# Performance work log

Hardware: AMD Instinct MI355X
Metric: run time of the kernel (lower is better)

The kernel has to match this reference:

```python
import jax, jax.numpy as jnp
import numpy as np

B, T, IN, H, OUT = 2048, 512, 6, 32, 64


def setup_inputs() -> dict:
    key = jax.random.key(0)
    ks = jax.random.split(key, 13)
    s_in = 1.0 / np.sqrt(H)  # torch LSTM/Linear default uniform bound
    u = lambda k, shape, s: jax.random.uniform(k, shape, jnp.float32, -s, s)
    return {
        "imu": jax.random.normal(ks[0], (B, T, IN), jnp.float32),
        # layer 0 (input_size=6)
        "w_ih0": u(ks[1], (4 * H, IN), s_in),
        "w_hh0": u(ks[2], (4 * H, H), s_in),
        "b_ih0": u(ks[3], (4 * H,), s_in),
        "b_hh0": u(ks[4], (4 * H,), s_in),
        # layer 1 (input_size=32)
        "w_ih1": u(ks[5], (4 * H, H), s_in),
        "w_hh1": u(ks[6], (4 * H, H), s_in),
        "b_ih1": u(ks[7], (4 * H,), s_in),
        "b_hh1": u(ks[8], (4 * H,), s_in),
        # heads
        "wf": u(ks[9], (OUT, H), s_in),
        "bf": u(ks[10], (OUT,), s_in),
        "wn": u(ks[11], (OUT, H), s_in),
        "bn": u(ks[12], (OUT,), s_in),
    }


def _lstm_layer(x, w_ih, w_hh, b_ih, b_hh):
    # x: [B, T, in] -> h sequence [B, T, H]; torch gate order: i, f, g, o
    b = x.shape[0]
    # precompute input contribution once: [B, T, 4H]
    gx = jnp.einsum("bti,gi->btg", x, w_ih) + b_ih + b_hh

    def step(carry, g_t):
        h, c = carry
        gates = g_t + h @ w_hh.T  # [B, 4H]
        i = jax.nn.sigmoid(gates[:, :H])
        f = jax.nn.sigmoid(gates[:, H:2 * H])
        g = jnp.tanh(gates[:, 2 * H:3 * H])
        o = jax.nn.sigmoid(gates[:, 3 * H:])
        c = f * c + i * g
        h = o * jnp.tanh(c)
        return (h, c), h

    h0 = jnp.zeros((b, H), x.dtype)
    (_, _), hs = jax.lax.scan(step, (h0, h0), jnp.swapaxes(gx, 0, 1))
    return jnp.swapaxes(hs, 0, 1)  # [B, T, H]


def reference(imu, w_ih0, w_hh0, b_ih0, b_hh0, w_ih1, w_hh1, b_ih1, b_hh1, wf, bf, wn, bn):
    h = _lstm_layer(imu, w_ih0, w_hh0, b_ih0, b_hh0)
    h = _lstm_layer(h, w_ih1, w_hh1, b_ih1, b_hh1)
    last = h[:, -1, :]  # [B, H]
    a_i = last @ wf.T + bf
    R_i = jnp.exp(last @ wn.T + bn)
    return (a_i, R_i)
```

## Files before the change

kernel.cpp:

```cpp
#include <hip/hip_runtime.h>

#define TT 512
#define BPB 8
#define NBLK (2048 / BPB)
#define OUTD 64

typedef __attribute__((ext_vector_type(8))) short short8;
typedef __attribute__((ext_vector_type(4))) float f32x4;

__device__ __forceinline__ short f2bf(float x) {
    union { float f; unsigned u; } v; v.f = x;
    unsigned r = (v.u + 0x7FFFu + ((v.u >> 16) & 1u)) >> 16;
    return (short)r;
}
__device__ __forceinline__ float sigm(float x) {
    return __builtin_amdgcn_rcpf(1.f + __expf(-x));
}
__device__ __forceinline__ float tanh_fast(float x) {
    return 2.f * sigm(2.f * x) - 1.f;
}

#define ACT_UPDATE(acc, c, hval)                                   \
    {                                                              \
        float gi = sigm((acc)[0]);                                 \
        float gf = sigm((acc)[1]);                                 \
        float gg = tanh_fast((acc)[2]);                            \
        float go = sigm((acc)[3]);                                 \
        (c) = gf * (c) + gi * gg;                                  \
        (hval) = go * tanh_fast((c));                              \
    }

__global__ __launch_bounds__(512, 1) void lstm2_inlane_kernel(
    const float* __restrict__ imu,
    const float* __restrict__ w_ih0, const float* __restrict__ w_hh0,
    const float* __restrict__ b_ih0, const float* __restrict__ b_hh0,
    const float* __restrict__ w_ih1, const float* __restrict__ w_hh1,
    const float* __restrict__ b_ih1, const float* __restrict__ b_hh1,
    const float* __restrict__ wf, const float* __restrict__ bf,
    const float* __restrict__ wn, const float* __restrict__ bn,
    float* __restrict__ out)
{
    const int tid   = threadIdx.x;
    const int l     = tid & 63;
    const int w     = tid >> 6;
    const int layer = w >> 2;
    const int pair  = w & 3;
    const int col   = l & 15;
    const int kg    = l >> 4;

    __shared__ __align__(16) short xfrag[TT][8][8];
    __shared__ __align__(16) short h1f[2][16][40];
    __shared__ __align__(16) short h2f[2][16][40];
    __shared__ __align__(16) float lasth[16][36];

    {
        short* p1 = &h1f[0][0][0];
        short* p2 = &h2f[0][0][0];
        for (int i = tid; i < 2 * 16 * 40; i += 512) { p1[i] = 0; p2[i] = 0; }
    }

    {
        const int bg0 = blockIdx.x * BPB;
        for (int p = tid; p < BPB * TT; p += 512) {
            const int b = p >> 9;
            const int t = p & (TT - 1);
            const float* src = imu + ((size_t)(bg0 + b) * TT + t) * 6;
            float2 a0 = *(const float2*)(src);
            float2 a1 = *(const float2*)(src + 2);
            float2 a2 = *(const float2*)(src + 4);
            unsigned* dst = (unsigned*)&xfrag[t][b][0];
            dst[0] = (unsigned short)f2bf(a0.x) | ((unsigned)(unsigned short)f2bf(a0.y) << 16);
            dst[1] = (unsigned short)f2bf(a1.x) | ((unsigned)(unsigned short)f2bf(a1.y) << 16);
            dst[2] = (unsigned short)f2bf(a2.x) | ((unsigned)(unsigned short)f2bf(a2.y) << 16);
            dst[3] = 0u;
        }
    }

    const int t0 = pair * 2, t1 = t0 + 1;
    const int m  = col;
    const int G0 = (m & 3) * 32 + t0 * 4 + (m >> 2);
    const int G1 = (m & 3) * 32 + t1 * 4 + (m >> 2);
    const int u0 = pair * 8 + kg;
    const int u1 = u0 + 4;

    short8 A00, A01, A10, A11;
    f32x4 bias0, bias1;
    if (layer == 0) {
        #pragma unroll
        for (int j = 0; j < 8; ++j) {
            A00[j] = (kg == 0 && j < 6) ? f2bf(w_ih0[G0 * 6 + j]) : (short)0;
            A10[j] = (kg == 0 && j < 6) ? f2bf(w_ih0[G1 * 6 + j]) : (short)0;
            A01[j] = f2bf(w_hh0[G0 * 32 + kg * 8 + j]);
            A11[j] = f2bf(w_hh0[G1 * 32 + kg * 8 + j]);
        }
        #pragma unroll
        for (int r = 0; r < 4; ++r) {
            bias0[r] = b_ih0[r * 32 + u0] + b_hh0[r * 32 + u0];
            bias1[r] = b_ih0[r * 32 + u1] + b_hh0[r * 32 + u1];
        }
    } else {
        #pragma unroll
        for (int j = 0; j < 8; ++j) {
            A00[j] = f2bf(w_ih1[G0 * 32 + kg * 8 + j]);
            A10[j] = f2bf(w_ih1[G1 * 32 + kg * 8 + j]);
            A01[j] = f2bf(w_hh1[G0 * 32 + kg * 8 + j]);
            A11[j] = f2bf(w_hh1[G1 * 32 + kg * 8 + j]);
        }
        #pragma unroll
        for (int r = 0; r < 4; ++r) {
            bias0[r] = b_ih1[r * 32 + u0] + b_hh1[r * 32 + u0];
            bias1[r] = b_ih1[r * 32 + u1] + b_hh1[r * 32 + u1];
        }
    }

    float c0 = 0.f, c1 = 0.f;

    const int xb = l & 7;
    const short8* h1r0  = (const short8*)&h1f[0][col][kg * 8];
    const short8* h1r1  = (const short8*)&h1f[1][col][kg * 8];
    const short8* h2r0  = (const short8*)&h2f[0][col][kg * 8];
    const short8* h2r1  = (const short8*)&h2f[1][col][kg * 8];

    __syncthreads();

    if (layer == 0) {
        short8 xv = *(const short8*)&xfrag[0][xb][0];
        f32x4 a0 = bias0, a1 = bias1;
        a0 = __builtin_amdgcn_mfma_f32_16x16x32_bf16(A00, xv, a0, 0, 0, 0);
        a1 = __builtin_amdgcn_mfma_f32_16x16x32_bf16(A10, xv, a1, 0, 0, 0);
        float h0, h1v;
        ACT_UPDATE(a0, c0, h0);
        ACT_UPDATE(a1, c1, h1v);
        h1f[1][col][u0] = f2bf(h0);
        h1f[1][col][u1] = f2bf(h1v);
    }
    __syncthreads();

#define STEP(T, H1R, H2R, WP)                                                   \
    {                                                                           \
        if (layer == 0) {                                                       \
            short8 xv = *(const short8*)&xfrag[(T) + 1][xb][0];                 \
            short8 hv = *(H1R);                                                 \
            f32x4 a0 = bias0, a1 = bias1;                                       \
            a0 = __builtin_amdgcn_mfma_f32_16x16x32_bf16(A00, xv, a0, 0, 0, 0); \
            a0 = __builtin_amdgcn_mfma_f32_16x16x32_bf16(A01, hv, a0, 0, 0, 0); \
            a1 = __builtin_amdgcn_mfma_f32_16x16x32_bf16(A10, xv, a1, 0, 0, 0); \
            a1 = __builtin_amdgcn_mfma_f32_16x16x32_bf16(A11, hv, a1, 0, 0, 0); \
            float h0, h1v;                                                      \
            ACT_UPDATE(a0, c0, h0);                                             \
            ACT_UPDATE(a1, c1, h1v);                                            \
            h1f[WP][col][u0] = f2bf(h0);                                        \
            h1f[WP][col][u1] = f2bf(h1v);                                       \
        } else {                                                                \
            short8 av = *(H1R);                                                 \
            short8 bv = *(H2R);                                                 \
            f32x4 a0 = bias0, a1 = bias1;                                       \
            a0 = __builtin_amdgcn_mfma_f32_16x16x32_bf16(A00, av, a0, 0, 0, 0); \
            a0 = __builtin_amdgcn_mfma_f32_16x16x32_bf16(A01, bv, a0, 0, 0, 0); \
            a1 = __builtin_amdgcn_mfma_f32_16x16x32_bf16(A10, av, a1, 0, 0, 0); \
            a1 = __builtin_amdgcn_mfma_f32_16x16x32_bf16(A11, bv, a1, 0, 0, 0); \
            float h0, h1v;                                                      \
            ACT_UPDATE(a0, c0, h0);                                             \
            ACT_UPDATE(a1, c1, h1v);                                            \
            h2f[WP][col][u0] = f2bf(h0);                                        \
            h2f[WP][col][u1] = f2bf(h1v);                                       \
        }                                                                       \
        __syncthreads();                                                        \
    }

    #pragma unroll 1
    for (int t = 0; t < TT - 2; t += 2) {
        STEP(t,     h1r1, h2r1, 0)
        STEP(t + 1, h1r0, h2r0, 1)
    }
    STEP(TT - 2, h1r1, h2r1, 0)

    if (layer == 1) {
        short8 av = *h1r0;
        short8 bv = *h2r0;
        f32x4 a0 = bias0, a1 = bias1;
        a0 = __builtin_amdgcn_mfma_f32_16x16x32_bf16(A00, av, a0, 0, 0, 0);
        a0 = __builtin_amdgcn_mfma_f32_16x16x32_bf16(A01, bv, a0, 0, 0, 0);
        a1 = __builtin_amdgcn_mfma_f32_16x16x32_bf16(A10, av, a1, 0, 0, 0);
        a1 = __builtin_amdgcn_mfma_f32_16x16x32_bf16(A11, bv, a1, 0, 0, 0);
        float h0, h1v;
        ACT_UPDATE(a0, c0, h0);
        ACT_UPDATE(a1, c1, h1v);
        lasth[col][u0] = h0;
        lasth[col][u1] = h1v;
    }
    __syncthreads();

    {
        const int b = tid >> 6;
        const int o = tid & 63;
        float accF = bf[o], accN = bn[o];
        const float4* wf4 = (const float4*)(wf + o * 32);
        const float4* wn4 = (const float4*)(wn + o * 32);
        const float4* hv4 = (const float4*)&lasth[b][0];
        #pragma unroll
        for (int k = 0; k < 8; ++k) {
            float4 h4 = hv4[k];
            float4 f4 = wf4[k];
            float4 n4 = wn4[k];
            accF += f4.x * h4.x + f4.y * h4.y + f4.z * h4.z + f4.w * h4.w;
            accN += n4.x * h4.x + n4.y * h4.y + n4.z * h4.z + n4.w * h4.w;
        }
        const size_t bg = (size_t)blockIdx.x * BPB + b;
        out[bg * OUTD + o] = accF;
        out[(size_t)2048 * OUTD + bg * OUTD + o] = __expf(accN);
    }
}

extern "C" void kernel_launch(void* const* d_in, const int* in_sizes, int n_in,
                              void* d_out, int out_size, void* d_ws, size_t ws_size,
                              hipStream_t stream) {
    const float* imu   = (const float*)d_in[0];
    const float* w_ih0 = (const float*)d_in[1];
    const float* w_hh0 = (const float*)d_in[2];
    const float* b_ih0 = (const float*)d_in[3];
    const float* b_hh0 = (const float*)d_in[4];
    const float* w_ih1 = (const float*)d_in[5];
    const float* w_hh1 = (const float*)d_in[6];
    const float* b_ih1 = (const float*)d_in[7];
    const float* b_hh1 = (const float*)d_in[8];
    const float* wf    = (const float*)d_in[9];
    const float* bf    = (const float*)d_in[10];
    const float* wn    = (const float*)d_in[11];
    const float* bn    = (const float*)d_in[12];
    float* out = (float*)d_out;

    lstm2_inlane_kernel<<<dim3(NBLK), dim3(512), 0, stream>>>(
        imu, w_ih0, w_hh0, b_ih0, b_hh0,
        w_ih1, w_hh1, b_ih1, b_hh1,
        wf, bf, wn, bn, out);
}
```

Measured before the change: 216.1 us.

## Permute hidden-state K layout to pack h stores, prefetch next x fragment

Each lane's two hidden outputs (u0, u1 = u0+4) are now stored as one packed bf16x2 write into adjacent shared-memory slots. The weight columns are permuted to match, so the MFMA reduction is unchanged. The next timestep's input fragment is loaded after the current step's store, hiding LDS latency before the barrier, and the x-dependent MFMAs are issued first. This halves LDS store instructions on the serial recurrence path. It relies on the epilogue code, not shown, reading h consistently with the new permuted layout.

```diff
diff --git a/kernel.cpp b/kernel.cpp
--- a/kernel.cpp
+++ b/kernel.cpp
@@ -1,4 +1,5 @@
 #include <hip/hip_runtime.h>
+#include <hip/hip_bf16.h>
 
 #define TT 512
 #define BPB 8
@@ -29,6 +30,11 @@
         (c) = gf * (c) + gi * gg;                                  \
         (hval) = go * tanh_fast((c));                              \
     }
+
+__device__ __forceinline__ int kperm(int s) {
+    int q = s & 7;
+    return (s & ~7) + (q >> 1) + ((q & 1) << 2);
+}
 
 __global__ __launch_bounds__(512, 1) void lstm2_inlane_kernel(
     const float* __restrict__ imu,
@@ -48,7 +54,7 @@
     const int col   = l & 15;
     const int kg    = l >> 4;
 
-    __shared__ __align__(16) short xfrag[TT][8][8];
+    __shared__ __align__(16) short xfrag[TT + 2][8][8];
     __shared__ __align__(16) short h1f[2][16][40];
     __shared__ __align__(16) short h2f[2][16][40];
     __shared__ __align__(16) float lasth[16][36];
@@ -82,16 +88,18 @@
     const int G1 = (m & 3) * 32 + t1 * 4 + (m >> 2);
     const int u0 = pair * 8 + kg;
     const int u1 = u0 + 4;
+    const int hslot = pair * 8 + kg * 2;
 
     short8 A00, A01, A10, A11;
     f32x4 bias0, bias1;
     if (layer == 0) {
         #pragma unroll
         for (int j = 0; j < 8; ++j) {
+            const int up = kg * 8 + (j >> 1) + ((j & 1) << 2);
             A00[j] = (kg == 0 && j < 6) ? f2bf(w_ih0[G0 * 6 + j]) : (short)0;
             A10[j] = (kg == 0 && j < 6) ? f2bf(w_ih0[G1 * 6 + j]) : (short)0;
-            A01[j] = f2bf(w_hh0[G0 * 32 + kg * 8 + j]);
-            A11[j] = f2bf(w_hh0[G1 * 32 + kg * 8 + j]);
+            A01[j] = f2bf(w_hh0[G0 * 32 + up]);
+            A11[j] = f2bf(w_hh0[G1 * 32 + up]);
         }
         #pragma unroll
         for (int r = 0; r < 4; ++r) {
@@ -101,10 +109,11 @@
     } else {
         #pragma unroll
         for (int j = 0; j < 8; ++j) {
-            A00[j] = f2bf(w_ih1[G0 * 32 + kg * 8 + j]);
-            A10[j] = f2bf(w_ih1[G1 * 32 + kg * 8 + j]);
-            A01[j] = f2bf(w_hh1[G0 * 32 + kg * 8 + j]);
-            A11[j] = f2bf(w_hh1[G1 * 32 + kg * 8 + j]);
+            const int up = kg * 8 + (j >> 1) + ((j & 1) << 2);
+            A00[j] = f2bf(w_ih1[G0 * 32 + up]);
+            A10[j] = f2bf(w_ih1[G1 * 32 + up]);
+            A01[j] = f2bf(w_hh1[G0 * 32 + up]);
+            A11[j] = f2bf(w_hh1[G1 * 32 + up]);
         }
         #pragma unroll
         for (int r = 0; r < 4; ++r) {
@@ -123,6 +132,7 @@
 
     __syncthreads();
 
+    short8 xv_cur;
     if (layer == 0) {
         short8 xv = *(const short8*)&xfrag[0][xb][0];
         f32x4 a0 = bias0, a1 = bias1;
@@ -131,26 +141,27 @@
         float h0, h1v;
         ACT_UPDATE(a0, c0, h0);
         ACT_UPDATE(a1, c1, h1v);
-        h1f[1][col][u0] = f2bf(h0);
-        h1f[1][col][u1] = f2bf(h1v);
+        *reinterpret_cast<__hip_bfloat162*>(&h1f[1][col][hslot]) =
+            __float22bfloat162_rn(make_float2(h0, h1v));
+        xv_cur = *(const short8*)&xfrag[1][xb][0];
     }
     __syncthreads();
 
 #define STEP(T, H1R, H2R, WP)                                                   \
     {                                                                           \
         if (layer == 0) {                                                       \
-            short8 xv = *(const short8*)&xfrag[(T) + 1][xb][0];                 \
             short8 hv = *(H1R);                                                 \
             f32x4 a0 = bias0, a1 = bias1;                                       \
-            a0 = __builtin_amdgcn_mfma_f32_16x16x32_bf16(A00, xv, a0, 0, 0, 0); \
+            a0 = __builtin_amdgcn_mfma_f32_16x16x32_bf16(A00, xv_cur, a0, 0, 0, 0); \
+            a1 = __builtin_amdgcn_mfma_f32_16x16x32_bf16(A10, xv_cur, a1, 0, 0, 0); \
             a0 = __builtin_amdgcn_mfma_f32_16x16x32_bf16(A01, hv, a0, 0, 0, 0); \
-            a1 = __builtin_amdgcn_mfma_f32_16x16x32_bf16(A10, xv, a1, 0, 0, 0); \
             a1 = __builtin_amdgcn_mfma_f32_16x16x32_bf16(A11, hv, a1, 0, 0, 0); \
             float h0, h1v;                                                      \
             ACT_UPDATE(a0, c0, h0);                                             \
             ACT_UPDATE(a1, c1, h1v);                                            \
-            h1f[WP][col][u0] = f2bf(h0);                                        \
-            h1f[WP][col][u1] = f2bf(h1v);                                       \
+            *reinterpret_cast<__hip_bfloat162*>(&h1f[WP][col][hslot]) =         \
+                __float22bfloat162_rn(make_float2(h0, h1v));                    \
+            xv_cur = *(const short8*)&xfrag[(T) + 2][xb][0];                    \
         } else {                                                                \
             short8 av = *(H1R);                                                 \
             short8 bv = *(H2R);                                                 \
@@ -162,8 +173,8 @@
             float h0, h1v;                                                      \
             ACT_UPDATE(a0, c0, h0);                                             \
             ACT_UPDATE(a1, c1, h1v);                                            \
-            h2f[WP][col][u0] = f2bf(h0);                                        \
-            h2f[WP][col][u1] = f2bf(h1v);                                       \
+            *reinterpret_cast<__hip_bfloat162*>(&h2f[WP][col][hslot]) =         \
+                __float22bfloat162_rn(make_float2(h0, h1v));                    \
         }                                                                       \
         __syncthreads();                                                        \
     }
```

Measured after the change: 199.3 us. 7.8% less time.

## Merge duplicate-column MFMA outputs via lane shuffle to halve activation work

Applied to the files above, without the earlier changes.

Only 8 of the 16 MFMA columns carry real batches, so lanes in the upper half were computing gate activations on padding. Each lane now pulls the second gate tile's results from lane^8 with a shuffle, so every lane runs one activation/cell update instead of two and writes a single h value. The x fragment for the next step is also prefetched from LDS one step ahead. The per-step activation work on the serial critical path shrinks, at the cost of four cross-lane shuffles per step and a slightly larger xfrag buffer.

```diff
diff --git a/kernel.cpp b/kernel.cpp
--- a/kernel.cpp
+++ b/kernel.cpp
@@ -1,4 +1,5 @@
 #include <hip/hip_runtime.h>
+#include <hip/hip_bf16.h>
 
 #define TT 512
 #define BPB 8
@@ -28,6 +29,15 @@
         float go = sigm((acc)[3]);                                 \
         (c) = gf * (c) + gi * gg;                                  \
         (hval) = go * tanh_fast((c));                              \
+    }
+
+#define MERGE(mg, a0, a1, colhi)                                   \
+    {                                                              \
+        _Pragma("unroll")                                          \
+        for (int r = 0; r < 4; ++r) {                              \
+            float s = __shfl_xor((a1)[r], 8);                      \
+            (mg)[r] = (colhi) ? s : (a0)[r];                       \
+        }                                                          \
     }
 
 __global__ __launch_bounds__(512, 1) void lstm2_inlane_kernel(
@@ -47,8 +57,10 @@
     const int pair  = w & 3;
     const int col   = l & 15;
     const int kg    = l >> 4;
-
-    __shared__ __align__(16) short xfrag[TT][8][8];
+    const bool colhi = (col >= 8);
+    const int batch  = col & 7;
+
+    __shared__ __align__(16) short xfrag[TT + 2][8][8];
     __shared__ __align__(16) short h1f[2][16][40];
     __shared__ __align__(16) short h2f[2][16][40];
     __shared__ __align__(16) float lasth[16][36];
@@ -82,6 +94,7 @@
     const int G1 = (m & 3) * 32 + t1 * 4 + (m >> 2);
     const int u0 = pair * 8 + kg;
     const int u1 = u0 + 4;
+    const int myunit = u0 + (colhi ? 4 : 0);
 
     short8 A00, A01, A10, A11;
     f32x4 bias0, bias1;
@@ -113,7 +126,7 @@
         }
     }
 
-    float c0 = 0.f, c1 = 0.f;
+    float c = 0.f;
 
     const int xb = l & 7;
     const short8* h1r0  = (const short8*)&h1f[0][col][kg * 8];
@@ -123,34 +136,36 @@
 
     __syncthreads();
 
+    short8 xv_cur;
     if (layer == 0) {
         short8 xv = *(const short8*)&xfrag[0][xb][0];
         f32x4 a0 = bias0, a1 = bias1;
         a0 = __builtin_amdgcn_mfma_f32_16x16x32_bf16(A00, xv, a0, 0, 0, 0);
         a1 = __builtin_amdgcn_mfma_f32_16x16x32_bf16(A10, xv, a1, 0, 0, 0);
-        float h0, h1v;
-        ACT_UPDATE(a0, c0, h0);
-        ACT_UPDATE(a1, c1, h1v);
-        h1f[1][col][u0] = f2bf(h0);
-        h1f[1][col][u1] = f2bf(h1v);
+        f32x4 mg;
+        MERGE(mg, a0, a1, colhi);
+        float h;
+        ACT_UPDATE(mg, c, h);
+        h1f[1][batch][myunit] = f2bf(h);
+        xv_cur = *(const short8*)&xfrag[1][xb][0];
     }
     __syncthreads();
 
 #define STEP(T, H1R, H2R, WP)                                                   \
     {                                                                           \
         if (layer == 0) {                                                       \
-            short8 xv = *(const short8*)&xfrag[(T) + 1][xb][0];                 \
             short8 hv = *(H1R);                                                 \
             f32x4 a0 = bias0, a1 = bias1;                                       \
-            a0 = __builtin_amdgcn_mfma_f32_16x16x32_bf16(A00, xv, a0, 0, 0, 0); \
+            a0 = __builtin_amdgcn_mfma_f32_16x16x32_bf16(A00, xv_cur, a0, 0, 0, 0); \
+            a1 = __builtin_amdgcn_mfma_f32_16x16x32_bf16(A10, xv_cur, a1, 0, 0, 0); \
             a0 = __builtin_amdgcn_mfma_f32_16x16x32_bf16(A01, hv, a0, 0, 0, 0); \
-            a1 = __builtin_amdgcn_mfma_f32_16x16x32_bf16(A10, xv, a1, 0, 0, 0); \
             a1 = __builtin_amdgcn_mfma_f32_16x16x32_bf16(A11, hv, a1, 0, 0, 0); \
-            float h0, h1v;                                                      \
-            ACT_UPDATE(a0, c0, h0);                                             \
-            ACT_UPDATE(a1, c1, h1v);                                            \
-            h1f[WP][col][u0] = f2bf(h0);                                        \
-            h1f[WP][col][u1] = f2bf(h1v);                                       \
+            f32x4 mg;                                                           \
+            MERGE(mg, a0, a1, colhi);                                           \
+            float h;                                                            \
+            ACT_UPDATE(mg, c, h);                                               \
+            h1f[WP][batch][myunit] = f2bf(h);                                   \
+            xv_cur = *(const short8*)&xfrag[(T) + 2][xb][0];                    \
         } else {                                                                \
             short8 av = *(H1R);                                                 \
             short8 bv = *(H2R);                                                 \
@@ -159,11 +174,11 @@
             a0 = __builtin_amdgcn_mfma_f32_16x16x32_bf16(A01, bv, a0, 0, 0, 0); \
             a1 = __builtin_amdgcn_mfma_f32_16x16x32_bf16(A10, av, a1, 0, 0, 0); \
             a1 = __builtin_amdgcn_mfma_f32_16x16x32_bf16(A11, bv, a1, 0, 0, 0); \
-            float h0, h1v;                                                      \
-            ACT_UPDATE(a0, c0, h0);                                             \
-            ACT_UPDATE(a1, c1, h1v);                                            \
-            h2f[WP][col][u0] = f2bf(h0);                                        \
-            h2f[WP][col][u1] = f2bf(h1v);                                       \
+            f32x4 mg;                                                           \
+            MERGE(mg, a0, a1, colhi);                                           \
+            float h;                                                            \
+            ACT_UPDATE(mg, c, h);                                               \
+            h2f[WP][batch][myunit] = f2bf(h);                                   \
         }                                                                       \
         __syncthreads();                                                        \
     }
@@ -183,11 +198,11 @@
         a0 = __builtin_amdgcn_mfma_f32_16x16x32_bf16(A01, bv, a0, 0, 0, 0);
         a1 = __builtin_amdgcn_mfma_f32_16x16x32_bf16(A10, av, a1, 0, 0, 0);
         a1 = __builtin_amdgcn_mfma_f32_16x16x32_bf16(A11, bv, a1, 0, 0, 0);
-        float h0, h1v;
-        ACT_UPDATE(a0, c0, h0);
-        ACT_UPDATE(a1, c1, h1v);
-        lasth[col][u0] = h0;
-        lasth[col][u1] = h1v;
+        f32x4 mg;
+        MERGE(mg, a0, a1, colhi);
+        float h;
+        ACT_UPDATE(mg, c, h);
+        lasth[batch][myunit] = h;
     }
     __syncthreads();
 
```

Result: faster. 174.2 us (-19.4%).
